# Performance work log

Measured on AMD Instinct MI355X. Metric: run time of the kernel, lower is better.

Reference implementation:

```python
import jax, jax.numpy as jnp
import numpy as np

B, T, D, H = 2, 2048, 1024, 16
HD = D // H  # head_dim = 64


def setup_inputs() -> dict:
    key = jax.random.key(0)
    ks = jax.random.split(key, 5)
    s = 0.02
    return {
        "x": jax.random.normal(ks[0], (B, T, D), dtype=jnp.float32),
        "Wqkv": jax.random.normal(ks[1], (3 * D, D), dtype=jnp.float32) * s,
        "bqkv": jax.random.normal(ks[2], (3 * D,), dtype=jnp.float32) * s,
        "Wproj": jax.random.normal(ks[3], (D, D), dtype=jnp.float32) * s,
        "bproj": jax.random.normal(ks[4], (D,), dtype=jnp.float32) * s,
    }


def reference(x, Wqkv, bqkv, Wproj, bproj):
    b, t, d = x.shape
    qkv = x @ Wqkv.T + bqkv                      # [B,T,3D]
    q, k, v = jnp.split(qkv, 3, axis=-1)
    # [B,T,D] -> [B,H,T,HD]
    def to_heads(u):
        return u.reshape(b, t, H, HD).transpose(0, 2, 1, 3)
    q, k, v = to_heads(q), to_heads(k), to_heads(v)
    scale = 1.0 / jnp.sqrt(jnp.float32(HD))
    attn = jnp.einsum("bhqd,bhkd->bhqk", q, k) * scale   # [B,H,T,T]
    causal = jnp.tril(jnp.ones((t, t), dtype=bool))
    attn = jnp.where(causal[None, None, :, :], attn, -jnp.inf)
    attn = jax.nn.softmax(attn, axis=-1)
    scores = jnp.einsum("bhqk,bhkd->bhqd", attn, v)       # [B,H,T,HD]
    scores = scores.transpose(0, 2, 1, 3).reshape(b, t, d)
    return scores @ Wproj.T + bproj
```

## Files before the change

### kernel.cpp

```cpp
#include <hip/hip_runtime.h>

typedef __bf16 bf16_8 __attribute__((ext_vector_type(8)));
typedef __bf16 bf16_4 __attribute__((ext_vector_type(4)));
typedef __bf16 bf16_2 __attribute__((ext_vector_type(2)));
typedef float  f32_4  __attribute__((ext_vector_type(4)));
typedef float  f32_16 __attribute__((ext_vector_type(16)));

typedef __attribute__((address_space(1))) const void* as1_cvp;
typedef __attribute__((address_space(3))) void*       as3_vp;

__device__ __forceinline__ void load16_to_lds(const void* g, void* l) {
    __builtin_amdgcn_global_load_lds((as1_cvp)g, (as3_vp)l, 16, 0, 0);
}

__device__ __forceinline__ float fast_exp2(float x) {
#if __has_builtin(__builtin_amdgcn_exp2f)
    return __builtin_amdgcn_exp2f(x);
#else
    return exp2f(x);
#endif
}

__device__ __forceinline__ unsigned pk2(float lo, float hi) {
    union { bf16_2 h; unsigned u; } t;
    t.h = bf16_2{(__bf16)lo, (__bf16)hi};
    return t.u;
}

__device__ __forceinline__ void pswap(unsigned &a, unsigned &b) {
    asm("v_permlane32_swap_b32 %0, %1" : "+v"(a), "+v"(b));
}

__global__ __launch_bounds__(256) void cvt_all(
    const float* __restrict__ a, const float* __restrict__ b,
    const float* __restrict__ c, __bf16* __restrict__ out,
    int na4, int nb4, int nc4)
{
    int i = blockIdx.x * 256 + threadIdx.x;
    if (i >= na4 + nb4 + nc4) return;
    float4 f;
    if (i < na4)            f = ((const float4*)a)[i];
    else if (i < na4 + nb4) f = ((const float4*)b)[i - na4];
    else                    f = ((const float4*)c)[i - na4 - nb4];
    bf16_4 v = { (__bf16)f.x, (__bf16)f.y, (__bf16)f.z, (__bf16)f.w };
    ((bf16_4*)out)[i] = v;
}

#define BM 128

template<int OUT_BF16, int BN_, int QKV, int PIPE>
__global__ __launch_bounds__(256) void gemm_bt(
    const __bf16* __restrict__ A,
    const __bf16* __restrict__ B,
    const float*  __restrict__ bias,
    __bf16* __restrict__ Cb, float* __restrict__ Cf,
    __bf16* __restrict__ Vtb,
    int M, int N, int K, int ldc)
{
    constexpr int NT   = BN_ / 32;
    constexpr int CSTR = BN_ + (OUT_BF16 ? 8 : 4);
    constexpr int BUFB = (128 * 64 + BN_ * 64) * 2;
    constexpr int SMEMSZ = PIPE ? (3 * BUFB) : 35840;
    __shared__ __align__(16) char smem[SMEMSZ];

    const int tid  = threadIdx.x;
    const int wave = tid >> 6;
    const int lane = tid & 63;
    const int wm = wave >> 1, wn = wave & 1;
    const int quad = lane >> 4, l16 = lane & 15;
    const int bm = blockIdx.y * BM, bn = blockIdx.x * BN_;

    const int r0 = tid >> 3;
    const int ch = tid & 7;
    const int cs = (ch ^ (r0 & 7)) * 8;

    f32_4 acc[4][NT];
    #pragma unroll
    for (int i = 0; i < 4; ++i)
        #pragma unroll
        for (int j = 0; j < NT; ++j)
            acc[i][j] = f32_4{0.f, 0.f, 0.f, 0.f};

    if constexpr (!PIPE) {
        __bf16* As = (__bf16*)smem;
        __bf16* Bs = As + 128 * 64;
        for (int k0 = 0; k0 < K; k0 += 64) {
            __syncthreads();
            #pragma unroll
            for (int p = 0; p < 4; ++p) {
                int row = p * 32 + r0;
                load16_to_lds(A + (size_t)(bm + row) * K + k0 + cs,
                              &As[(p * 32 + wave * 8) * 64]);
            }
            #pragma unroll
            for (int p = 0; p < BN_ / 32; ++p) {
                int row = p * 32 + r0;
                load16_to_lds(B + (size_t)(bn + row) * K + k0 + cs,
                              &Bs[(p * 32 + wave * 8) * 64]);
            }
            __syncthreads();

            #pragma unroll
            for (int h = 0; h < 2; ++h) {
                const int sl = ((quad + h * 4) ^ (l16 & 7)) * 8;
                bf16_8 af[4], bfr[NT];
                #pragma unroll
                for (int mt = 0; mt < 4; ++mt)
                    af[mt] = *(const bf16_8*)&As[(wm * 64 + mt * 16 + l16) * 64 + sl];
                #pragma unroll
                for (int nt = 0; nt < NT; ++nt)
                    bfr[nt] = *(const bf16_8*)&Bs[(wn * (BN_/2) + nt * 16 + l16) * 64 + sl];
                #pragma unroll
                for (int mt = 0; mt < 4; ++mt)
                    #pragma unroll
                    for (int nt = 0; nt < NT; ++nt)
                        acc[mt][nt] = __builtin_amdgcn_mfma_f32_16x16x32_bf16(
                            af[mt], bfr[nt], acc[mt][nt], 0, 0, 0);
            }
        }
    } else {
        const int nit = K / 64;
        #pragma unroll
        for (int t = 0; t < 2; ++t) {
            __bf16* AsT = (__bf16*)(smem + t * BUFB);
            __bf16* BsT = AsT + 128 * 64;
            #pragma unroll
            for (int p = 0; p < 4; ++p)
                load16_to_lds(A + (size_t)(bm + p * 32 + r0) * K + t * 64 + cs,
                              &AsT[(p * 32 + wave * 8) * 64]);
            #pragma unroll
            for (int p = 0; p < BN_ / 32; ++p)
                load16_to_lds(B + (size_t)(bn + p * 32 + r0) * K + t * 64 + cs,
                              &BsT[(p * 32 + wave * 8) * 64]);
        }
        int cur = 0, sb = 2;
        for (int j = 0; j < nit; ++j) {
            if (j < nit - 1) asm volatile("s_waitcnt vmcnt(6)" ::: "memory");
            else             asm volatile("s_waitcnt vmcnt(0)" ::: "memory");
            __builtin_amdgcn_s_barrier();

            if (j + 2 < nit) {
                const int k0 = (j + 2) * 64;
                __bf16* AsT = (__bf16*)(smem + sb * BUFB);
                __bf16* BsT = AsT + 128 * 64;
                #pragma unroll
                for (int p = 0; p < 4; ++p)
                    load16_to_lds(A + (size_t)(bm + p * 32 + r0) * K + k0 + cs,
                                  &AsT[(p * 32 + wave * 8) * 64]);
                #pragma unroll
                for (int p = 0; p < BN_ / 32; ++p)
                    load16_to_lds(B + (size_t)(bn + p * 32 + r0) * K + k0 + cs,
                                  &BsT[(p * 32 + wave * 8) * 64]);
            }

            __bf16* As = (__bf16*)(smem + cur * BUFB);
            __bf16* Bs = As + 128 * 64;
            #pragma unroll
            for (int h = 0; h < 2; ++h) {
                const int sl = ((quad + h * 4) ^ (l16 & 7)) * 8;
                bf16_8 af[4], bfr[NT];
                #pragma unroll
                for (int mt = 0; mt < 4; ++mt)
                    af[mt] = *(const bf16_8*)&As[(wm * 64 + mt * 16 + l16) * 64 + sl];
                #pragma unroll
                for (int nt = 0; nt < NT; ++nt)
                    bfr[nt] = *(const bf16_8*)&Bs[(wn * (BN_/2) + nt * 16 + l16) * 64 + sl];
                #pragma unroll
                for (int mt = 0; mt < 4; ++mt)
                    #pragma unroll
                    for (int nt = 0; nt < NT; ++nt)
                        acc[mt][nt] = __builtin_amdgcn_mfma_f32_16x16x32_bf16(
                            af[mt], bfr[nt], acc[mt][nt], 0, 0, 0);
            }
            cur = (cur == 2) ? 0 : cur + 1;
            sb  = (sb  == 2) ? 0 : sb  + 1;
        }
    }

    if (QKV && bn >= 2048) {
        const int b_ = bm >> 11;
        const int t0 = (bm & 2047) + wm * 64;
        #pragma unroll
        for (int nt = 0; nt < NT; ++nt) {
            int vrow = (bn - 2048) + wn * (BN_/2) + nt * 16 + l16;
            float bv = bias ? bias[2048 + vrow] : 0.f;
            #pragma unroll
            for (int mt = 0; mt < 4; ++mt) {
                bf16_4 ov;
                #pragma unroll
                for (int r = 0; r < 4; ++r)
                    ov[r] = (__bf16)(acc[mt][nt][r] + bv);
                *(bf16_4*)(Vtb + ((size_t)b_ * 1024 + vrow) * 2048
                           + t0 + mt * 16 + quad * 4) = ov;
            }
        }
        return;
    }

    __syncthreads();

    if (OUT_BF16) {
        __bf16* Cs = (__bf16*)smem;
        #pragma unroll
        for (int mt = 0; mt < 4; ++mt)
            #pragma unroll
            for (int nt = 0; nt < NT; ++nt) {
                int col = wn * (BN_/2) + nt * 16 + l16;
                float bv = bias ? bias[bn + col] : 0.f;
                #pragma unroll
                for (int r = 0; r < 4; ++r)
                    Cs[(wm * 64 + mt * 16 + quad * 4 + r) * CSTR + col] =
                        (__bf16)(acc[mt][nt][r] + bv);
            }
        __syncthreads();
        const int rr = tid >> 4, cc = (tid & 15) * 8;
        #pragma unroll
        for (int p = 0; p < 8; ++p) {
            int row = p * 16 + rr;
            bf16_8 v = *(const bf16_8*)&Cs[row * CSTR + cc];
            *(bf16_8*)(Cb + (size_t)(bm + row) * ldc + bn + cc) = v;
        }
    } else {
        float* Cs = (float*)smem;
        #pragma unroll
        for (int mt = 0; mt < 4; ++mt)
            #pragma unroll
            for (int nt = 0; nt < NT; ++nt) {
                int col = wn * (BN_/2) + nt * 16 + l16;
                float bv = bias ? bias[bn + col] : 0.f;
                #pragma unroll
                for (int r = 0; r < 4; ++r)
                    Cs[(wm * 64 + mt * 16 + quad * 4 + r) * CSTR + col] =
                        acc[mt][nt][r] + bv;
            }
        __syncthreads();
        const int rr = tid >> 4, cc = (tid & 15) * 4;
        #pragma unroll
        for (int p = 0; p < 8; ++p) {
            int row = p * 16 + rr;
            float4 v = *(const float4*)&Cs[row * CSTR + cc];
            *(float4*)(Cf + (size_t)(bm + row) * ldc + bn + cc) = v;
        }
    }
}

__global__ __launch_bounds__(256, 2) void attn_kernel(
    const __bf16* __restrict__ qk, const __bf16* __restrict__ vt,
    __bf16* __restrict__ out,
    float* __restrict__ opart, float* __restrict__ lpart)
{
    constexpr int T = 2048;
    __shared__ __align__(16) char pool[65536];
    __bf16* Ks = (__bf16*)pool;
    float*  Om = (float*)pool;
    float*  Lm = (float*)(pool + 34816);

    const int tid  = threadIdx.x;
    const int wave = tid >> 6;
    const int lane = tid & 63;
    const int wq = wave & 1, wg = wave >> 1;
    const int l32 = lane & 31, hh = lane >> 5;

    const int fid = blockIdx.x;
    const int xcd = fid & 7;
    const int u   = fid >> 3;
    const int bh  = xcd * 4 + (u & 3);
    const int typ = u >> 2;
    const int b = bh >> 4, h = bh & 15;

    int qt, t0, t1, sidx;
    bool direct;
    if (typ < 16) {
        int qa = 7 - (typ >> 1);
        sidx = typ & 1;
        qt = 8 + qa;
        int half0 = (qt + 2) >> 1;
        t0 = sidx ? half0 : 0;
        t1 = sidx ? (qt + 1) : half0;
        direct = false;
    } else {
        qt = 23 - typ;
        sidx = 0;
        t0 = 0; t1 = qt + 1;
        direct = true;
    }

    const size_t rowbase = (size_t)b * T;
    const __bf16* Kbase = qk + 1024 + h * 64;
    const __bf16* Vbase = vt + (size_t)bh * 64 * 2048;

    const int sr   = tid >> 3;
    const int schf = (tid & 7) ^ (sr & 7);

    constexpr float QSCALE = 0.125f * 1.4426950408889634f;
    bf16_8 aq[2][4];
    #pragma unroll
    for (int qq = 0; qq < 2; ++qq)
        #pragma unroll
        for (int df = 0; df < 4; ++df) {
            const __bf16* qp = qk + (rowbase + qt*128 + wq*64 + qq*32 + l32)*2048
                               + h*64 + df*16 + hh*8;
            bf16_8 v = *(const bf16_8*)qp;
            #pragma unroll
            for (int u2 = 0; u2 < 8; ++u2) v[u2] = (__bf16)((float)v[u2] * QSCALE);
            aq[qq][df] = v;
        }

    #pragma unroll
    for (int sub = 0; sub < 2; ++sub)
        #pragma unroll
        for (int p = 0; p < 2; ++p) {
            load16_to_lds(Kbase + (rowbase + t0*128 + sub*64 + sr + 32*p)*2048 + schf*8,
                          Ks + sub*4096 + p*2048 + wave*512);
            load16_to_lds(Vbase + (size_t)(sr + 32*p)*2048 + t0*128 + sub*64 + schf*8,
                          Ks + 8192 + sub*4096 + p*2048 + wave*512);
        }

    f32_16 O[2][2];
    #pragma unroll
    for (int dt = 0; dt < 2; ++dt)
        #pragma unroll
        for (int qq = 0; qq < 2; ++qq)
            #pragma unroll
            for (int r = 0; r < 16; ++r) O[dt][qq][r] = 0.f;
    float l_i[2] = {0.f, 0.f};

    const int krow = wg*32 + l32;
    const int ksw  = krow & 7;

    for (int j = t0; j < t1; ++j) {
        const int cur = (j - t0) & 1, nxt = cur ^ 1;
        asm volatile("s_waitcnt vmcnt(0)" ::: "memory");
        __builtin_amdgcn_s_barrier();

        if (j + 1 < t1) {
            const int jn = j + 1;
            #pragma unroll
            for (int sub = 0; sub < 2; ++sub)
                #pragma unroll
                for (int p = 0; p < 2; ++p) {
                    load16_to_lds(Kbase + (rowbase + jn*128 + sub*64 + sr + 32*p)*2048 + schf*8,
                                  Ks + nxt*16384 + sub*4096 + p*2048 + wave*512);
                    load16_to_lds(Vbase + (size_t)(sr + 32*p)*2048 + jn*128 + sub*64 + schf*8,
                                  Ks + nxt*16384 + 8192 + sub*4096 + p*2048 + wave*512);
                }
        }

        const bool diag = (j == qt);
        #pragma unroll
        for (int s2 = 0; s2 < 2; ++s2) {
            const __bf16* Kc = Ks + cur*16384 + s2*4096;
            const __bf16* Vc = Ks + cur*16384 + 8192 + s2*4096;

            f32_16 S[2];
            __builtin_amdgcn_s_setprio(1);
            bf16_8 kf[4];
            #pragma unroll
            for (int df = 0; df < 4; ++df)
                kf[df] = *(const bf16_8*)&Kc[krow*64 + (((2*df + hh) ^ ksw) << 3)];
            #pragma unroll
            for (int qq = 0; qq < 2; ++qq) {
                f32_16 z;
                #pragma unroll
                for (int r = 0; r < 16; ++r) z[r] = 0.f;
                #pragma unroll
                for (int df = 0; df < 4; ++df)
                    z = __builtin_amdgcn_mfma_f32_32x32x16_bf16(kf[df], aq[qq][df], z, 0, 0, 0);
                S[qq] = z;
            }
            __builtin_amdgcn_s_setprio(0);

            unsigned fr[2][8];
            #pragma unroll
            for (int qq = 0; qq < 2; ++qq) {
                float pe[16];
                const int qg = qt*128 + wq*64 + qq*32 + l32;
                #pragma unroll
                for (int r = 0; r < 16; ++r) {
                    float e = fast_exp2(S[qq][r]);
                    if (diag) {
                        int key = j*128 + s2*64 + wg*32 + (r&3) + 8*(r>>2) + 4*hh;
                        if (key > qg) e = 0.f;
                    }
                    pe[r] = e;
                    l_i[qq] += e;
                }
                unsigned A = pk2(pe[0],  pe[1]),  Bv = pk2(pe[2],  pe[3]),
                         C = pk2(pe[4],  pe[5]),  D  = pk2(pe[6],  pe[7]),
                         E = pk2(pe[8],  pe[9]),  F  = pk2(pe[10], pe[11]),
                         G = pk2(pe[12], pe[13]), H  = pk2(pe[14], pe[15]);
                pswap(A, C); pswap(Bv, D); pswap(E, G); pswap(F, H);
                fr[qq][0] = A; fr[qq][1] = Bv; fr[qq][2] = C; fr[qq][3] = D;
                fr[qq][4] = E; fr[qq][5] = F;  fr[qq][6] = G; fr[qq][7] = H;
            }

            __builtin_amdgcn_s_setprio(1);
            #pragma unroll
            for (int kh = 0; kh < 2; ++kh) {
                #pragma unroll
                for (int dt = 0; dt < 2; ++dt) {
                    const int d = dt*32 + l32;
                    bf16_8 vf = *(const bf16_8*)&Vc[d*64 +
                                    (((wg*4 + kh*2 + hh) ^ (d & 7)) << 3)];
                    #pragma unroll
                    for (int qq = 0; qq < 2; ++qq) {
                        union { unsigned dw[4]; bf16_8 v; } u2;
                        u2.dw[0] = fr[qq][kh*4+0]; u2.dw[1] = fr[qq][kh*4+1];
                        u2.dw[2] = fr[qq][kh*4+2]; u2.dw[3] = fr[qq][kh*4+3];
                        O[dt][qq] = __builtin_amdgcn_mfma_f32_32x32x16_bf16(
                            vf, u2.v, O[dt][qq], 0, 0, 0);
                    }
                }
            }
            __builtin_amdgcn_s_setprio(0);
        }
    }

    float lw[2];
    #pragma unroll
    for (int qq = 0; qq < 2; ++qq) {
        float v = l_i[qq];
        v += __shfl_xor(v, 32, 64);
        lw[qq] = v;
    }

    __syncthreads();
    if (wg == 1) {
        #pragma unroll
        for (int qq = 0; qq < 2; ++qq) {
            const int qrow = wq*64 + qq*32 + l32;
            #pragma unroll
            for (int dt = 0; dt < 2; ++dt)
                #pragma unroll
                for (int g = 0; g < 4; ++g) {
                    f32_4 t = { O[dt][qq][g*4+0], O[dt][qq][g*4+1],
                                O[dt][qq][g*4+2], O[dt][qq][g*4+3] };
                    *(f32_4*)&Om[qrow*68 + dt*32 + g*8 + hh*4] = t;
                }
            if (hh == 0) Lm[qrow] = lw[qq];
        }
    }
    __syncthreads();
    if (wg == 0) {
        #pragma unroll
        for (int qq = 0; qq < 2; ++qq) {
            const int qrow = wq*64 + qq*32 + l32;
            const float lsum = lw[qq] + Lm[qrow];
            if (direct) {
                const float inv = 1.f / lsum;
                const size_t obase = (rowbase + qt*128 + qrow) * 1024 + h*64;
                #pragma unroll
                for (int dt = 0; dt < 2; ++dt)
                    #pragma unroll
                    for (int g = 0; g < 4; ++g) {
                        f32_4 o2 = *(const f32_4*)&Om[qrow*68 + dt*32 + g*8 + hh*4];
                        bf16_4 ov;
                        #pragma unroll
                        for (int r = 0; r < 4; ++r)
                            ov[r] = (__bf16)((O[dt][qq][g*4+r] + o2[r]) * inv);
                        *(bf16_4*)(out + obase + dt*32 + g*8 + hh*4) = ov;
                    }
            } else {
                const size_t pb = ((size_t)(bh*8 + (qt-8))*2 + sidx) * 8192
                                  + (size_t)qrow * 64;
                #pragma unroll
                for (int dt = 0; dt < 2; ++dt)
                    #pragma unroll
                    for (int g = 0; g < 4; ++g) {
                        f32_4 o2 = *(const f32_4*)&Om[qrow*68 + dt*32 + g*8 + hh*4];
                        f32_4 s;
                        #pragma unroll
                        for (int r = 0; r < 4; ++r)
                            s[r] = O[dt][qq][g*4+r] + o2[r];
                        *(f32_4*)&opart[pb + dt*32 + g*8 + hh*4] = s;
                    }
                if (hh == 0)
                    lpart[((bh*8 + (qt-8))*2 + sidx) * 128 + qrow] = lsum;
            }
        }
    }
}

__global__ __launch_bounds__(256) void attn_merge(
    const float* __restrict__ opart, const float* __restrict__ lpart,
    __bf16* __restrict__ out)
{
    const int t  = blockIdx.x;
    const int bh = t >> 3, qa = t & 7, qt = 8 + qa;
    const int b = bh >> 4, h = bh & 15;
    const int tid = threadIdx.x;
    const int rr = tid >> 4;
    const int cc = (tid & 15) * 4;
    const size_t p0 = (size_t)(t*2 + 0) * 8192;
    const size_t p1 = (size_t)(t*2 + 1) * 8192;
    #pragma unroll
    for (int p = 0; p < 8; ++p) {
        const int row = p * 16 + rr;
        const float inv = 1.f / (lpart[(t*2)*128 + row] + lpart[(t*2+1)*128 + row]);
        f32_4 a = *(const f32_4*)&opart[p0 + row*64 + cc];
        f32_4 c = *(const f32_4*)&opart[p1 + row*64 + cc];
        bf16_4 ov;
        #pragma unroll
        for (int r = 0; r < 4; ++r)
            ov[r] = (__bf16)((a[r] + c[r]) * inv);
        *(bf16_4*)(out + ((size_t)b*2048 + qt*128 + row)*1024 + h*64 + cc) = ov;
    }
}

extern "C" void kernel_launch(void* const* d_in, const int* in_sizes, int n_in,
                              void* d_out, int out_size, void* d_ws, size_t ws_size,
                              hipStream_t stream)
{
    constexpr int Bc = 2, Tc = 2048, Dc = 1024;
    constexpr int M  = Bc * Tc;
    constexpr int N1 = 3 * Dc;

    const float* x     = (const float*)d_in[0];
    const float* Wqkv  = (const float*)d_in[1];
    const float* bqkv  = (const float*)d_in[2];
    const float* Wproj = (const float*)d_in[3];
    const float* bproj = (const float*)d_in[4];
    float* outp = (float*)d_out;

    __bf16* xb     = (__bf16*)d_ws;
    __bf16* wqkvb  = xb     + (size_t)M * Dc;
    __bf16* wprojb = wqkvb  + (size_t)N1 * Dc;
    __bf16* qkb    = wprojb + (size_t)Dc * Dc;
    __bf16* vtb    = qkb    + (size_t)M * 2048;
    __bf16* attnb  = vtb    + (size_t)Bc * 1024 * 2048;
    float*  opart  = (float*)(attnb + (size_t)M * Dc);
    float*  lpart  = opart + (size_t)256 * 2 * 8192;

    {
        int na4 = M * Dc / 4, nb4 = N1 * Dc / 4, nc4 = Dc * Dc / 4;
        int n4 = na4 + nb4 + nc4;
        cvt_all<<<(n4 + 255) / 256, 256, 0, stream>>>(x, Wqkv, Wproj, xb, na4, nb4, nc4);
    }

    gemm_bt<1, 128, 1, 0><<<dim3(N1 / 128, M / BM), 256, 0, stream>>>(
        xb, wqkvb, bqkv, qkb, nullptr, vtb, M, N1, Dc, 2048);

    attn_kernel<<<dim3(768), 256, 0, stream>>>(qkb, vtb, attnb, opart, lpart);
    attn_merge<<<dim3(256), 256, 0, stream>>>(opart, lpart, attnb);

    gemm_bt<0, 64, 0, 1><<<dim3(Dc / 64, M / BM), 256, 0, stream>>>(
        attnb, wprojb, bproj, nullptr, outp, nullptr, M, Dc, Dc, Dc);
}
```

Measured before the change: 182.3 us.

## Rebalance causal attention work into 512 equal-cost blocks with paired segments

Replaces the 768-block schedule (split long query tiles plus separate short direct tiles) with 512 blocks. Role-0 blocks process the first 8 key tiles of a long query tile. Role-1 blocks process the remaining keys of that tile and then a short direct query tile, so every block does about 9 key tiles. The aim is to even out per-block work and cut tail imbalance and launch granularity across CUs. The cost is an extra segment loop with additional barriers and reloading Q/K for a second tile within one block.

```diff
diff --git a/kernel.cpp b/kernel.cpp
--- a/kernel.cpp
+++ b/kernel.cpp
@@ -261,29 +261,13 @@
     const int wq = wave & 1, wg = wave >> 1;
     const int l32 = lane & 31, hh = lane >> 5;
 
-    const int fid = blockIdx.x;
-    const int xcd = fid & 7;
-    const int u   = fid >> 3;
-    const int bh  = xcd * 4 + (u & 3);
-    const int typ = u >> 2;
+    const int fid  = blockIdx.x;
+    const int xcd  = fid & 7;
+    const int role = fid >> 8;
+    const int w    = (fid >> 3) & 31;
+    const int p    = w >> 2;
+    const int bh   = xcd * 4 + (w & 3);
     const int b = bh >> 4, h = bh & 15;
-
-    int qt, t0, t1, sidx;
-    bool direct;
-    if (typ < 16) {
-        int qa = 7 - (typ >> 1);
-        sidx = typ & 1;
-        qt = 8 + qa;
-        int half0 = (qt + 2) >> 1;
-        t0 = sidx ? half0 : 0;
-        t1 = sidx ? (qt + 1) : half0;
-        direct = false;
-    } else {
-        qt = 23 - typ;
-        sidx = 0;
-        t0 = 0; t1 = qt + 1;
-        direct = true;
-    }
 
     const size_t rowbase = (size_t)b * T;
     const __bf16* Kbase = qk + 1024 + h * 64;
@@ -293,191 +277,208 @@
     const int schf = (tid & 7) ^ (sr & 7);
 
     constexpr float QSCALE = 0.125f * 1.4426950408889634f;
-    bf16_8 aq[2][4];
-    #pragma unroll
-    for (int qq = 0; qq < 2; ++qq)
-        #pragma unroll
-        for (int df = 0; df < 4; ++df) {
-            const __bf16* qp = qk + (rowbase + qt*128 + wq*64 + qq*32 + l32)*2048
-                               + h*64 + df*16 + hh*8;
-            bf16_8 v = *(const bf16_8*)qp;
-            #pragma unroll
-            for (int u2 = 0; u2 < 8; ++u2) v[u2] = (__bf16)((float)v[u2] * QSCALE);
-            aq[qq][df] = v;
-        }
-
-    #pragma unroll
-    for (int sub = 0; sub < 2; ++sub)
-        #pragma unroll
-        for (int p = 0; p < 2; ++p) {
-            load16_to_lds(Kbase + (rowbase + t0*128 + sub*64 + sr + 32*p)*2048 + schf*8,
-                          Ks + sub*4096 + p*2048 + wave*512);
-            load16_to_lds(Vbase + (size_t)(sr + 32*p)*2048 + t0*128 + sub*64 + schf*8,
-                          Ks + 8192 + sub*4096 + p*2048 + wave*512);
-        }
-
-    f32_16 O[2][2];
-    #pragma unroll
-    for (int dt = 0; dt < 2; ++dt)
-        #pragma unroll
-        for (int qq = 0; qq < 2; ++qq)
-            #pragma unroll
-            for (int r = 0; r < 16; ++r) O[dt][qq][r] = 0.f;
-    float l_i[2] = {0.f, 0.f};
-
     const int krow = wg*32 + l32;
     const int ksw  = krow & 7;
-
-    for (int j = t0; j < t1; ++j) {
-        const int cur = (j - t0) & 1, nxt = cur ^ 1;
-        asm volatile("s_waitcnt vmcnt(0)" ::: "memory");
-        __builtin_amdgcn_s_barrier();
-
-        if (j + 1 < t1) {
-            const int jn = j + 1;
-            #pragma unroll
-            for (int sub = 0; sub < 2; ++sub)
-                #pragma unroll
-                for (int p = 0; p < 2; ++p) {
-                    load16_to_lds(Kbase + (rowbase + jn*128 + sub*64 + sr + 32*p)*2048 + schf*8,
-                                  Ks + nxt*16384 + sub*4096 + p*2048 + wave*512);
-                    load16_to_lds(Vbase + (size_t)(sr + 32*p)*2048 + jn*128 + sub*64 + schf*8,
-                                  Ks + nxt*16384 + 8192 + sub*4096 + p*2048 + wave*512);
+    const int nseg = role ? 2 : 1;
+
+    for (int sg = 0; sg < nseg; ++sg) {
+        int qt, t0, t1, sidx;
+        bool direct;
+        if (sg == 0) {
+            qt = p + 8; sidx = role;
+            t0 = role ? 8 : 0;
+            t1 = role ? (p + 9) : 8;
+            direct = false;
+        } else {
+            qt = 7 - p; sidx = 0;
+            t0 = 0; t1 = 8 - p;
+            direct = true;
+        }
+
+        bf16_8 aq[2][4];
+        #pragma unroll
+        for (int qq = 0; qq < 2; ++qq)
+            #pragma unroll
+            for (int df = 0; df < 4; ++df) {
+                const __bf16* qp = qk + (rowbase + qt*128 + wq*64 + qq*32 + l32)*2048
+                                   + h*64 + df*16 + hh*8;
+                bf16_8 v = *(const bf16_8*)qp;
+                #pragma unroll
+                for (int u2 = 0; u2 < 8; ++u2) v[u2] = (__bf16)((float)v[u2] * QSCALE);
+                aq[qq][df] = v;
+            }
+
+        #pragma unroll
+        for (int sub = 0; sub < 2; ++sub)
+            #pragma unroll
+            for (int pp = 0; pp < 2; ++pp) {
+                load16_to_lds(Kbase + (rowbase + t0*128 + sub*64 + sr + 32*pp)*2048 + schf*8,
+                              Ks + sub*4096 + pp*2048 + wave*512);
+                load16_to_lds(Vbase + (size_t)(sr + 32*pp)*2048 + t0*128 + sub*64 + schf*8,
+                              Ks + 8192 + sub*4096 + pp*2048 + wave*512);
+            }
+
+        f32_16 O[2][2];
+        #pragma unroll
+        for (int dt = 0; dt < 2; ++dt)
+            #pragma unroll
+            for (int qq = 0; qq < 2; ++qq)
+                #pragma unroll
+                for (int r = 0; r < 16; ++r) O[dt][qq][r] = 0.f;
+        float l_i[2] = {0.f, 0.f};
+
+        for (int j = t0; j < t1; ++j) {
+            const int cur = (j - t0) & 1, nxt = cur ^ 1;
+            asm volatile("s_waitcnt vmcnt(0)" ::: "memory");
+            __builtin_amdgcn_s_barrier();
+
+            if (j + 1 < t1) {
+                const int jn = j + 1;
+                #pragma unroll
+                for (int sub = 0; sub < 2; ++sub)
+                    #pragma unroll
+                    for (int pp = 0; pp < 2; ++pp) {
+                        load16_to_lds(Kbase + (rowbase + jn*128 + sub*64 + sr + 32*pp)*2048 + schf*8,
+                                      Ks + nxt*16384 + sub*4096 + pp*2048 + wave*512);
+                        load16_to_lds(Vbase + (size_t)(sr + 32*pp)*2048 + jn*128 + sub*64 + schf*8,
+                                      Ks + nxt*16384 + 8192 + sub*4096 + pp*2048 + wave*512);
+                    }
+            }
+
+            const bool diag = (j == qt);
+            #pragma unroll
+            for (int s2 = 0; s2 < 2; ++s2) {
+                const __bf16* Kc = Ks + cur*16384 + s2*4096;
+                const __bf16* Vc = Ks + cur*16384 + 8192 + s2*4096;
+
+                f32_16 S[2];
+                __builtin_amdgcn_s_setprio(1);
+                bf16_8 kf[4];
+                #pragma unroll
+                for (int df = 0; df < 4; ++df)
+                    kf[df] = *(const bf16_8*)&Kc[krow*64 + (((2*df + hh) ^ ksw) << 3)];
+                #pragma unroll
+                for (int qq = 0; qq < 2; ++qq) {
+                    f32_16 z;
+                    #pragma unroll
+                    for (int r = 0; r < 16; ++r) z[r] = 0.f;
+                    #pragma unroll
+                    for (int df = 0; df < 4; ++df)
+                        z = __builtin_amdgcn_mfma_f32_32x32x16_bf16(kf[df], aq[qq][df], z, 0, 0, 0);
+                    S[qq] = z;
                 }
-        }
-
-        const bool diag = (j == qt);
-        #pragma unroll
-        for (int s2 = 0; s2 < 2; ++s2) {
-            const __bf16* Kc = Ks + cur*16384 + s2*4096;
-            const __bf16* Vc = Ks + cur*16384 + 8192 + s2*4096;
-
-            f32_16 S[2];
-            __builtin_amdgcn_s_setprio(1);
-            bf16_8 kf[4];
-            #pragma unroll
-            for (int df = 0; df < 4; ++df)
-                kf[df] = *(const bf16_8*)&Kc[krow*64 + (((2*df + hh) ^ ksw) << 3)];
-            #pragma unroll
-            for (int qq = 0; qq < 2; ++qq) {
-                f32_16 z;
-                #pragma unroll
-                for (int r = 0; r < 16; ++r) z[r] = 0.f;
-                #pragma unroll
-                for (int df = 0; df < 4; ++df)
-                    z = __builtin_amdgcn_mfma_f32_32x32x16_bf16(kf[df], aq[qq][df], z, 0, 0, 0);
-                S[qq] = z;
-            }
-            __builtin_amdgcn_s_setprio(0);
-
-            unsigned fr[2][8];
-            #pragma unroll
-            for (int qq = 0; qq < 2; ++qq) {
-                float pe[16];
-                const int qg = qt*128 + wq*64 + qq*32 + l32;
-                #pragma unroll
-                for (int r = 0; r < 16; ++r) {
-                    float e = fast_exp2(S[qq][r]);
-                    if (diag) {
-                        int key = j*128 + s2*64 + wg*32 + (r&3) + 8*(r>>2) + 4*hh;
-                        if (key > qg) e = 0.f;
+                __builtin_amdgcn_s_setprio(0);
+
+                unsigned fr[2][8];
+                #pragma unroll
+                for (int qq = 0; qq < 2; ++qq) {
+                    float pe[16];
+                    const int qg = qt*128 + wq*64 + qq*32 + l32;
+                    #pragma unroll
+                    for (int r = 0; r < 16; ++r) {
+                        float e = fast_exp2(S[qq][r]);
+                        if (diag) {
+                            int key = j*128 + s2*64 + wg*32 + (r&3) + 8*(r>>2) + 4*hh;
+                            if (key > qg) e = 0.f;
+                        }
+                        pe[r] = e;
+                        l_i[qq] += e;
                     }
-                    pe[r] = e;
-                    l_i[qq] += e;
+                    unsigned A = pk2(pe[0],  pe[1]),  Bv = pk2(pe[2],  pe[3]),
+                             C = pk2(pe[4],  pe[5]),  D  = pk2(pe[6],  pe[7]),
+                             E = pk2(pe[8],  pe[9]),  F  = pk2(pe[10], pe[11]),
+                             G = pk2(pe[12], pe[13]), H  = pk2(pe[14], pe[15]);
+                    pswap(A, C); pswap(Bv, D); pswap(E, G); pswap(F, H);
+                    fr[qq][0] = A; fr[qq][1] = Bv; fr[qq][2] = C; fr[qq][3] = D;
+                    fr[qq][4] = E; fr[qq][5] = F;  fr[qq][6] = G; fr[qq][7] = H;
                 }
-                unsigned A = pk2(pe[0],  pe[1]),  Bv = pk2(pe[2],  pe[3]),
-                         C = pk2(pe[4],  pe[5]),  D  = pk2(pe[6],  pe[7]),
-                         E = pk2(pe[8],  pe[9]),  F  = pk2(pe[10], pe[11]),
-                         G = pk2(pe[12], pe[13]), H  = pk2(pe[14], pe[15]);
-                pswap(A, C); pswap(Bv, D); pswap(E, G); pswap(F, H);
-                fr[qq][0] = A; fr[qq][1] = Bv; fr[qq][2] = C; fr[qq][3] = D;
-                fr[qq][4] = E; fr[qq][5] = F;  fr[qq][6] = G; fr[qq][7] = H;
-            }
-
-            __builtin_amdgcn_s_setprio(1);
-            #pragma unroll
-            for (int kh = 0; kh < 2; ++kh) {
-                #pragma unroll
-                for (int dt = 0; dt < 2; ++dt) {
-                    const int d = dt*32 + l32;
-                    bf16_8 vf = *(const bf16_8*)&Vc[d*64 +
-                                    (((wg*4 + kh*2 + hh) ^ (d & 7)) << 3)];
-                    #pragma unroll
-                    for (int qq = 0; qq < 2; ++qq) {
-                        union { unsigned dw[4]; bf16_8 v; } u2;
-                        u2.dw[0] = fr[qq][kh*4+0]; u2.dw[1] = fr[qq][kh*4+1];
-                        u2.dw[2] = fr[qq][kh*4+2]; u2.dw[3] = fr[qq][kh*4+3];
-                        O[dt][qq] = __builtin_amdgcn_mfma_f32_32x32x16_bf16(
-                            vf, u2.v, O[dt][qq], 0, 0, 0);
+
+                __builtin_amdgcn_s_setprio(1);
+                #pragma unroll
+                for (int kh = 0; kh < 2; ++kh) {
+                    #pragma unroll
+                    for (int dt = 0; dt < 2; ++dt) {
+                        const int d = dt*32 + l32;
+                        bf16_8 vf = *(const bf16_8*)&Vc[d*64 +
+                                        (((wg*4 + kh*2 + hh) ^ (d & 7)) << 3)];
+                        #pragma unroll
+                        for (int qq = 0; qq < 2; ++qq) {
+                            union { unsigned dw[4]; bf16_8 v; } u2;
+                            u2.dw[0] = fr[qq][kh*4+0]; u2.dw[1] = fr[qq][kh*4+1];
+                            u2.dw[2] = fr[qq][kh*4+2]; u2.dw[3] = fr[qq][kh*4+3];
+                            O[dt][qq] = __builtin_amdgcn_mfma_f32_32x32x16_bf16(
+                                vf, u2.v, O[dt][qq], 0, 0, 0);
+                        }
                     }
                 }
-            }
-            __builtin_amdgcn_s_setprio(0);
-        }
-    }
-
-    float lw[2];
-    #pragma unroll
-    for (int qq = 0; qq < 2; ++qq) {
-        float v = l_i[qq];
-        v += __shfl_xor(v, 32, 64);
-        lw[qq] = v;
-    }
-
-    __syncthreads();
-    if (wg == 1) {
+                __builtin_amdgcn_s_setprio(0);
+            }
+        }
+
+        float lw[2];
         #pragma unroll
         for (int qq = 0; qq < 2; ++qq) {
-            const int qrow = wq*64 + qq*32 + l32;
-            #pragma unroll
-            for (int dt = 0; dt < 2; ++dt)
-                #pragma unroll
-                for (int g = 0; g < 4; ++g) {
-                    f32_4 t = { O[dt][qq][g*4+0], O[dt][qq][g*4+1],
-                                O[dt][qq][g*4+2], O[dt][qq][g*4+3] };
-                    *(f32_4*)&Om[qrow*68 + dt*32 + g*8 + hh*4] = t;
+            float v = l_i[qq];
+            v += __shfl_xor(v, 32, 64);
+            lw[qq] = v;
+        }
+
+        __syncthreads();
+        if (wg == 1) {
+            #pragma unroll
+            for (int qq = 0; qq < 2; ++qq) {
+                const int qrow = wq*64 + qq*32 + l32;
+                #pragma unroll
+                for (int dt = 0; dt < 2; ++dt)
+                    #pragma unroll
+                    for (int g = 0; g < 4; ++g) {
+                        f32_4 t = { O[dt][qq][g*4+0], O[dt][qq][g*4+1],
+                                    O[dt][qq][g*4+2], O[dt][qq][g*4+3] };
+                        *(f32_4*)&Om[qrow*68 + dt*32 + g*8 + hh*4] = t;
+                    }
+                if (hh == 0) Lm[qrow] = lw[qq];
+            }
+        }
+        __syncthreads();
+        if (wg == 0) {
+            #pragma unroll
+            for (int qq = 0; qq < 2; ++qq) {
+                const int qrow = wq*64 + qq*32 + l32;
+                const float lsum = lw[qq] + Lm[qrow];
+                if (direct) {
+                    const float inv = 1.f / lsum;
+                    const size_t obase = (rowbase + qt*128 + qrow) * 1024 + h*64;
+                    #pragma unroll
+                    for (int dt = 0; dt < 2; ++dt)
+                        #pragma unroll
+                        for (int g = 0; g < 4; ++g) {
+                            f32_4 o2 = *(const f32_4*)&Om[qrow*68 + dt*32 + g*8 + hh*4];
+                            bf16_4 ov;
+                            #pragma unroll
+                            for (int r = 0; r < 4; ++r)
+                                ov[r] = (__bf16)((O[dt][qq][g*4+r] + o2[r]) * inv);
+                            *(bf16_4*)(out + obase + dt*32 + g*8 + hh*4) = ov;
+                        }
+                } else {
+                    const size_t pb = ((size_t)(bh*8 + (qt-8))*2 + sidx) * 8192
+                                      + (size_t)qrow * 64;
+                    #pragma unroll
+                    for (int dt = 0; dt < 2; ++dt)
+                        #pragma unroll
+                        for (int g = 0; g < 4; ++g) {
+                            f32_4 o2 = *(const f32_4*)&Om[qrow*68 + dt*32 + g*8 + hh*4];
+                            f32_4 s;
+                            #pragma unroll
+                            for (int r = 0; r < 4; ++r)
+                                s[r] = O[dt][qq][g*4+r] + o2[r];
+                            *(f32_4*)&opart[pb + dt*32 + g*8 + hh*4] = s;
+                        }
+                    if (hh == 0)
+                        lpart[((bh*8 + (qt-8))*2 + sidx) * 128 + qrow] = lsum;
                 }
-            if (hh == 0) Lm[qrow] = lw[qq];
-        }
-    }
-    __syncthreads();
-    if (wg == 0) {
-        #pragma unroll
-        for (int qq = 0; qq < 2; ++qq) {
-            const int qrow = wq*64 + qq*32 + l32;
-            const float lsum = lw[qq] + Lm[qrow];
-            if (direct) {
-                const float inv = 1.f / lsum;
-                const size_t obase = (rowbase + qt*128 + qrow) * 1024 + h*64;
-                #pragma unroll
-                for (int dt = 0; dt < 2; ++dt)
-                    #pragma unroll
-                    for (int g = 0; g < 4; ++g) {
-                        f32_4 o2 = *(const f32_4*)&Om[qrow*68 + dt*32 + g*8 + hh*4];
-                        bf16_4 ov;
-                        #pragma unroll
-                        for (int r = 0; r < 4; ++r)
-                            ov[r] = (__bf16)((O[dt][qq][g*4+r] + o2[r]) * inv);
-                        *(bf16_4*)(out + obase + dt*32 + g*8 + hh*4) = ov;
-                    }
-            } else {
-                const size_t pb = ((size_t)(bh*8 + (qt-8))*2 + sidx) * 8192
-                                  + (size_t)qrow * 64;
-                #pragma unroll
-                for (int dt = 0; dt < 2; ++dt)
-                    #pragma unroll
-                    for (int g = 0; g < 4; ++g) {
-                        f32_4 o2 = *(const f32_4*)&Om[qrow*68 + dt*32 + g*8 + hh*4];
-                        f32_4 s;
-                        #pragma unroll
-                        for (int r = 0; r < 4; ++r)
-                            s[r] = O[dt][qq][g*4+r] + o2[r];
-                        *(f32_4*)&opart[pb + dt*32 + g*8 + hh*4] = s;
-                    }
-                if (hh == 0)
-                    lpart[((bh*8 + (qt-8))*2 + sidx) * 128 + qrow] = lsum;
-            }
-        }
+            }
+        }
+        __syncthreads();
     }
 }
 
@@ -540,7 +541,7 @@
     gemm_bt<1, 128, 1, 0><<<dim3(N1 / 128, M / BM), 256, 0, stream>>>(
         xb, wqkvb, bqkv, qkb, nullptr, vtb, M, N1, Dc, 2048);
 
-    attn_kernel<<<dim3(768), 256, 0, stream>>>(qkb, vtb, attnb, opart, lpart);
+    attn_kernel<<<dim3(512), 256, 0, stream>>>(qkb, vtb, attnb, opart, lpart);
     attn_merge<<<dim3(256), 256, 0, stream>>>(opart, lpart, attnb);
 
     gemm_bt<0, 64, 0, 1><<<dim3(Dc / 64, M / BM), 256, 0, stream>>>(
```

After: 172.4 us. 5.4% less time.
